# Kernel optimization log

Measured on AMD Instinct MI355X. Metric: run time of the kernel, lower is better.

## Reference

```python
import jax, jax.numpy as jnp
import numpy as np

B, L, D, HD, DC = 2, 2048, 2048, 64, 2048
NH = D // HD  # 32 heads


def _rms_norm(x, eps):
    return x * jax.lax.rsqrt(jnp.mean(jnp.square(x), axis=-1, keepdims=True) + eps)


def _apply_rope(x, rope):
    # x: [b,h,l,d]; rope: [2,l,d]. x_hat = interleave(-x_odd, x_even)
    x2 = x.reshape(*x.shape[:-1], HD // 2, 2)
    x_hat = jnp.stack([-x2[..., 1], x2[..., 0]], axis=-1).reshape(x.shape)
    return x * rope[0] + x_hat * rope[1]


def setup_inputs() -> dict:
    key = jax.random.key(0)
    ks = jax.random.split(key, 6)
    return {
        "x": jax.random.normal(ks[0], (B, L, D), jnp.float32),
        "condition": jax.random.normal(ks[1], (B, DC), jnp.float32),
        "rope": jax.random.normal(ks[2], (2, L, HD), jnp.float32),
        "w_ada": jax.random.normal(ks[3], (2 * D, DC), jnp.float32) * 0.02,
        "w_qkv": jax.random.normal(ks[4], (3 * D, D), jnp.float32) * 0.02,
        "w_out": jax.random.normal(ks[5], (D, D), jnp.float32) * 0.02,
        "qk_w": jnp.ones((HD,), jnp.float32),
    }


def reference(x, condition, rope, w_ada, w_qkv, w_out, qk_w):
    eps = jnp.finfo(x.dtype).eps
    # AdaRMSNorm
    ss = (condition @ w_ada.T)[:, None, :]          # [b,1,2D]
    shift, scale = jnp.split(ss, 2, axis=-1)
    h = _rms_norm(x, eps) * (1.0 + scale) + shift   # [b,l,D]
    # fused QKV projection: 'b l (n h d)'
    qkv = (h @ w_qkv.T).reshape(B, L, 3, NH, HD)
    qkv = jnp.transpose(qkv, (2, 0, 3, 1, 4))       # [3,b,h,l,d]
    q, k, v = qkv[0], qkv[1], qkv[2]
    # per-head RMSNorm (with affine weight) + RoPE
    q = _apply_rope(_rms_norm(q, eps) * qk_w, rope)
    k = _apply_rope(_rms_norm(k, eps) * qk_w, rope)
    # SDPA
    scores = jnp.einsum('bhqd,bhkd->bhqk', q, k) / jnp.sqrt(jnp.asarray(HD, x.dtype))
    attn = jax.nn.softmax(scores, axis=-1)
    o = jnp.einsum('bhqk,bhkd->bhqd', attn, v)      # [b,h,l,d]
    o = jnp.transpose(o, (0, 2, 1, 3)).reshape(B, L, D)
    return o @ w_out.T
```

## Files before the change

kernel.cpp:

```cpp
#include <hip/hip_runtime.h>


typedef __bf16 bf16x8 __attribute__((ext_vector_type(8)));
typedef float  f32x4  __attribute__((ext_vector_type(4)));
typedef float  f32x16 __attribute__((ext_vector_type(16)));

#define EPS_F32 1.1920929e-07f
#define QSCALE 0.18033688011112042f

#if defined(__has_builtin)
#  if __has_builtin(__builtin_amdgcn_exp2f)
#    define EXP2F(x) __builtin_amdgcn_exp2f(x)
#  else
#    define EXP2F(x) __expf((x) * 0.6931471805599453f)
#  endif
#  if __has_builtin(__builtin_amdgcn_rcpf)
#    define RCPF(x) __builtin_amdgcn_rcpf(x)
#  else
#    define RCPF(x) (1.0f / (x))
#  endif
#else
#  define EXP2F(x) __expf((x) * 0.6931471805599453f)
#  define RCPF(x) (1.0f / (x))
#endif

__device__ __forceinline__ float bf2f(unsigned int u16) {
  union { unsigned int i; float f; } v; v.i = (u16 & 0xffffu) << 16; return v.f;
}
__device__ __forceinline__ unsigned short f2bf(float f) {
  union { float f; unsigned int i; } v; v.f = f;
  unsigned int r = v.i + 0x7fffu + ((v.i >> 16) & 1u);
  return (unsigned short)(r >> 16);
}
__device__ __forceinline__ unsigned int f2bf_rn_u(float f) {
  union { float f; unsigned int i; } v; v.f = f;
  return v.i + 0x8000u;
}

__device__ __forceinline__ void gload16(const void* g, void* l) {
  __builtin_amdgcn_global_load_lds(
      (const __attribute__((address_space(1))) unsigned int*)(unsigned long long)g,
      (__attribute__((address_space(3))) unsigned int*)(unsigned int)(unsigned long long)l,
      16, 0, 0);
}

__global__ __launch_bounds__(256) void ada_gemm_kernel(
    const float* __restrict__ cond, const float* __restrict__ w_ada,
    float* __restrict__ ss)
{
  const int lane = threadIdx.x & 63;
  const int gw = blockIdx.x * 4 + (threadIdx.x >> 6);
  const int b = gw >> 12;
  const int j = gw & 4095;
  const float4* wr = (const float4*)(w_ada + j * 2048);
  const float4* cr = (const float4*)(cond + b * 2048);
  float acc = 0.f;
  #pragma unroll
  for (int k4 = 0; k4 < 8; ++k4) {
    float4 w = wr[lane + k4 * 64];
    float4 c = cr[lane + k4 * 64];
    acc += w.x * c.x + w.y * c.y + w.z * c.z + w.w * c.w;
  }
  #pragma unroll
  for (int off = 1; off < 64; off <<= 1) acc += __shfl_xor(acc, off);
  if (lane == 0) ss[b * 4096 + j] = acc;
}

__global__ __launch_bounds__(256) void ada_rms_kernel(
    const float* __restrict__ x, const float* __restrict__ ss,
    unsigned short* __restrict__ H)
{
  const int row = blockIdx.x;
  const int b = row >> 11;
  const int tid = threadIdx.x;
  const int lane = tid & 63, wave = tid >> 6;
  const float* xr = x + (size_t)row * 2048;
  float4 v0 = ((const float4*)xr)[tid * 2];
  float4 v1 = ((const float4*)xr)[tid * 2 + 1];
  float ssq = v0.x*v0.x + v0.y*v0.y + v0.z*v0.z + v0.w*v0.w
            + v1.x*v1.x + v1.y*v1.y + v1.z*v1.z + v1.w*v1.w;
  #pragma unroll
  for (int off = 1; off < 64; off <<= 1) ssq += __shfl_xor(ssq, off);
  __shared__ float red[4];
  if (lane == 0) red[wave] = ssq;
  __syncthreads();
  const float tot = red[0] + red[1] + red[2] + red[3];
  const float r = rsqrtf(tot * (1.f / 2048.f) + EPS_F32);
  const int c0 = tid * 8;
  const float* sh = ss + b * 4096;
  float xv[8] = {v0.x, v0.y, v0.z, v0.w, v1.x, v1.y, v1.z, v1.w};
  unsigned int pk[4];
  #pragma unroll
  for (int p = 0; p < 4; ++p) {
    const int c = c0 + p * 2;
    float h0 = xv[p*2+0] * r * (1.f + sh[2048 + c])     + sh[c];
    float h1 = xv[p*2+1] * r * (1.f + sh[2048 + c + 1]) + sh[c + 1];
    pk[p] = (unsigned int)f2bf(h0) | ((unsigned int)f2bf(h1) << 16);
  }
  *(uint4*)&H[(size_t)row * 2048 + c0] = make_uint4(pk[0], pk[1], pk[2], pk[3]);
}

__global__ __launch_bounds__(256) void cast2_kernel(
    const float* __restrict__ a,
    const float* __restrict__ b,
    unsigned short* __restrict__ dst)
{
  const int i = blockIdx.x * 256 + threadIdx.x;
  float4 v = (i < 3145728) ? ((const float4*)a)[i]
                           : ((const float4*)b)[i - 3145728];
  unsigned int p0 = (unsigned int)f2bf(v.x) | ((unsigned int)f2bf(v.y) << 16);
  unsigned int p1 = (unsigned int)f2bf(v.z) | ((unsigned int)f2bf(v.w) << 16);
  *(uint2*)&dst[(size_t)i * 4] = make_uint2(p0, p1);
}

template <int MODE>
__global__ __launch_bounds__(256) void gemm_bt_kernel(
    const unsigned short* __restrict__ A,
    const unsigned short* __restrict__ Bw,
    void* __restrict__ Cv,
    unsigned short* __restrict__ vt,
    int M, int N, int K)
{
  __shared__ unsigned short As[128 * 32];
  __shared__ unsigned short Bs[128 * 32];
  const int tid  = threadIdx.x;
  const int lane = tid & 63;
  const int wave = tid >> 6;
  const int wm = (wave >> 1) * 64;
  const int wn = (wave & 1) * 64;
  const int bm = blockIdx.y * 128;
  const int bn = blockIdx.x * 128;

  f32x4 acc[4][4] = {};

  const int sm = tid >> 2;
  const int sk = (tid & 3) * 8;
  const unsigned short* Ap  = A  + (size_t)(bm + sm) * K + sk;
  const unsigned short* Ap2 = Ap + (size_t)64 * K;
  const unsigned short* Bp  = Bw + (size_t)(bn + sm) * K + sk;
  const unsigned short* Bp2 = Bp + (size_t)64 * K;
  unsigned short* lA  = &As[tid * 8];
  unsigned short* lA2 = &As[tid * 8 + 2048];
  unsigned short* lB  = &Bs[tid * 8];
  unsigned short* lB2 = &Bs[tid * 8 + 2048];

  const int fr = lane & 15;
  const int fk = (lane >> 4) * 8;

  for (int k0 = 0; k0 < K; k0 += 32) {
    __syncthreads();
    gload16(Ap  + k0, lA);
    gload16(Ap2 + k0, lA2);
    gload16(Bp  + k0, lB);
    gload16(Bp2 + k0, lB2);
    __syncthreads();

    bf16x8 af[4], bfr[4];
    #pragma unroll
    for (int i = 0; i < 4; ++i)
      af[i] = *(const bf16x8*)&As[(wm + i * 16 + fr) * 32 + fk];
    #pragma unroll
    for (int j = 0; j < 4; ++j)
      bfr[j] = *(const bf16x8*)&Bs[(wn + j * 16 + fr) * 32 + fk];
    #pragma unroll
    for (int i = 0; i < 4; ++i)
      #pragma unroll
      for (int j = 0; j < 4; ++j)
        acc[i][j] = __builtin_amdgcn_mfma_f32_16x16x32_bf16(af[i], bfr[j], acc[i][j], 0, 0, 0);
  }

  const int cr = (lane >> 4) * 4;
  const int cc = lane & 15;
  if (MODE == 2 && bn >= 4096) {
    #pragma unroll
    for (int i = 0; i < 4; ++i)
      #pragma unroll
      for (int j = 0; j < 4; ++j)
        #pragma unroll
        for (int r = 0; r < 4; ++r) {
          const int m  = bm + wm + i * 16 + cr + r;
          const int dg = bn + wn + j * 16 + cc - 4096;
          const int l  = m & 2047;
          const size_t dst = ((size_t)((m >> 11) * 32 + (dg >> 6)) * 64 + (dg & 63)) * 2048
                           + (l >> 6) * 64 + (l & 15) * 4 + ((l >> 4) & 3);
          vt[dst] = f2bf(acc[i][j][r]);
        }
  } else {
    #pragma unroll
    for (int i = 0; i < 4; ++i)
      #pragma unroll
      for (int j = 0; j < 4; ++j)
        #pragma unroll
        for (int r = 0; r < 4; ++r) {
          const int row = bm + wm + i * 16 + cr + r;
          const int col = bn + wn + j * 16 + cc;
          if (MODE != 0)
            ((unsigned short*)Cv)[(size_t)row * N + col] = f2bf(acc[i][j][r]);
          else
            ((float*)Cv)[(size_t)row * N + col] = acc[i][j][r];
        }
  }
}

__global__ __launch_bounds__(256) void qk_rope_kernel(
    unsigned short* __restrict__ QKV, const float* __restrict__ rope,
    const float* __restrict__ qk_w)
{
  const int lane = threadIdx.x & 63;
  const int gid = blockIdx.x * 4 + (threadIdx.x >> 6);
  const int l = gid & 2047;
  const int h = (gid >> 11) & 31;
  const int b = gid >> 16;
  const int base = (b * 2048 + l) * 6144 + h * 64 + lane;
  const float r0 = rope[l * 64 + lane];
  const float r1 = rope[131072 + l * 64 + lane];
  const float w  = qk_w[lane];
  #pragma unroll
  for (int t = 0; t < 2; ++t) {
    const int idx = base + 2048 * t;
    const float v = bf2f(QKV[idx]);
    float sq = v * v;
    #pragma unroll
    for (int off = 1; off < 64; off <<= 1) sq += __shfl_xor(sq, off);
    const float vn = v * rsqrtf(sq * (1.f / 64.f) + EPS_F32) * w;
    const float vp = __shfl_xor(vn, 1);
    const float vh = (lane & 1) ? vp : -vp;
    const float scale = (t == 0) ? QSCALE : 1.0f;
    QKV[idx] = f2bf((vn * r0 + vh * r1) * scale);
  }
}

__global__ __launch_bounds__(256, 2) void attn_mfma_kernel(
    const unsigned short* __restrict__ QKV,
    const unsigned short* __restrict__ Vt,
    unsigned short* __restrict__ O)
{
  __shared__ unsigned short Ks[64 * 72];
  __shared__ unsigned short Vs[64 * 72];
  __shared__ unsigned short Ps[4 * 64 * 68];
  const int tid  = threadIdx.x;
  const int lane = tid & 63;
  const int wave = tid >> 6;
  const int blk = blockIdx.x;
  const int bh = blk & 63;
  const int qt = blk >> 6;
  const int b = bh >> 5, h = bh & 31;
  const int rowbase = b << 11;
  const int qbase = qt * 256 + wave * 64;

  const int m16  = lane & 15;
  const int quad = lane >> 4;
  const int m32  = lane & 31;
  const int hl   = lane >> 5;

  bf16x8 qf[4][2];
  #pragma unroll
  for (int qi = 0; qi < 4; ++qi)
    #pragma unroll
    for (int ch = 0; ch < 2; ++ch)
      qf[qi][ch] = *(const bf16x8*)&QKV[(size_t)(rowbase + qbase + qi * 16 + m16) * 6144
                                        + h * 64 + ch * 32 + quad * 8];

  const int sr = tid >> 2;
  const int sc = (tid & 3) * 16;
  const unsigned short* Kg = QKV + (size_t)(rowbase + sr) * 6144 + 2048 + h * 64 + sc;
  const unsigned short* Vg = Vt + (size_t)(bh * 64 + sr) * 2048 + sc;

  f32x16 accO[2][2] = {};
  float part[4][4] = {};
  unsigned short* Pw = &Ps[(wave * 64) * 68];

  for (int kt = 0; kt < 32; ++kt) {
    __syncthreads();
    {
      const uint4* kp = (const uint4*)(Kg + (size_t)kt * 64 * 6144);
      const uint4* vp = (const uint4*)(Vg + kt * 64);
      uint4 k0 = kp[0], k1 = kp[1];
      uint4 v0 = vp[0], v1 = vp[1];
      *(uint4*)&Ks[sr * 72 + sc]     = k0;
      *(uint4*)&Ks[sr * 72 + sc + 8] = k1;
      *(uint4*)&Vs[sr * 72 + sc]     = v0;
      *(uint4*)&Vs[sr * 72 + sc + 8] = v1;
    }
    __syncthreads();

    unsigned int pk[4][4][2];
    #pragma unroll
    for (int kj = 0; kj < 4; ++kj) {
      bf16x8 kf0 = *(const bf16x8*)&Ks[(kj * 16 + m16) * 72 + quad * 8];
      bf16x8 kf1 = *(const bf16x8*)&Ks[(kj * 16 + m16) * 72 + 32 + quad * 8];
      #pragma unroll
      for (int qi = 0; qi < 4; ++qi) {
        f32x4 acc = {};
        acc = __builtin_amdgcn_mfma_f32_16x16x32_bf16(qf[qi][0], kf0, acc, 0, 0, 0);
        acc = __builtin_amdgcn_mfma_f32_16x16x32_bf16(qf[qi][1], kf1, acc, 0, 0, 0);
        #pragma unroll
        for (int r = 0; r < 4; ++r) {
          float p = EXP2F(acc[r]);
          part[qi][r] += p;
          unsigned int pb = f2bf_rn_u(p);
          if (kj == 0)      pk[qi][r][0]  = pb >> 16;
          else if (kj == 1) pk[qi][r][0] |= pb & 0xffff0000u;
          else if (kj == 2) pk[qi][r][1]  = pb >> 16;
          else              pk[qi][r][1] |= pb & 0xffff0000u;
        }
      }
    }
    #pragma unroll
    for (int qi = 0; qi < 4; ++qi)
      #pragma unroll
      for (int r = 0; r < 4; ++r)
        *(uint2*)&Pw[(qi * 16 + quad * 4 + r) * 68 + m16 * 4] =
            make_uint2(pk[qi][r][0], pk[qi][r][1]);

    #pragma unroll
    for (int ch = 0; ch < 4; ++ch) {
      bf16x8 pa0 = *(const bf16x8*)&Pw[m32 * 68 + ch * 16 + hl * 8];
      bf16x8 pa1 = *(const bf16x8*)&Pw[(32 + m32) * 68 + ch * 16 + hl * 8];
      bf16x8 vb0 = *(const bf16x8*)&Vs[m32 * 72 + ch * 16 + hl * 8];
      bf16x8 vb1 = *(const bf16x8*)&Vs[(32 + m32) * 72 + ch * 16 + hl * 8];
      accO[0][0] = __builtin_amdgcn_mfma_f32_32x32x16_bf16(pa0, vb0, accO[0][0], 0, 0, 0);
      accO[0][1] = __builtin_amdgcn_mfma_f32_32x32x16_bf16(pa0, vb1, accO[0][1], 0, 0, 0);
      accO[1][0] = __builtin_amdgcn_mfma_f32_32x32x16_bf16(pa1, vb0, accO[1][0], 0, 0, 0);
      accO[1][1] = __builtin_amdgcn_mfma_f32_32x32x16_bf16(pa1, vb1, accO[1][1], 0, 0, 0);
    }
  }

  #pragma unroll
  for (int qi = 0; qi < 4; ++qi)
    #pragma unroll
    for (int r = 0; r < 4; ++r)
      #pragma unroll
      for (int off = 1; off < 16; off <<= 1)
        part[qi][r] += __shfl_xor(part[qi][r], off);

  #pragma unroll
  for (int qs = 0; qs < 2; ++qs) {
    #pragma unroll
    for (int reg = 0; reg < 16; ++reg) {
      const int r = reg & 3;
      const int s = reg >> 2;
      const int qsrc = ((2 * s + hl) & 3) * 16 + m16;
      const float rs = __shfl(part[qs * 2 + (reg >> 3)][r], qsrc);
      const float inv = RCPF(rs);
      const int rho = r + 8 * s + 4 * hl;
      const size_t base = (size_t)(rowbase + qbase + qs * 32 + rho) * 2048 + h * 64;
      O[base + m32]      = f2bf(accO[qs][0][reg] * inv);
      O[base + 32 + m32] = f2bf(accO[qs][1][reg] * inv);
    }
  }
}

extern "C" void kernel_launch(void* const* d_in, const int* in_sizes, int n_in,
                              void* d_out, int out_size, void* d_ws, size_t ws_size,
                              hipStream_t stream) {
  (void)in_sizes; (void)n_in; (void)out_size; (void)ws_size;
  const float* x     = (const float*)d_in[0];
  const float* cond  = (const float*)d_in[1];
  const float* rope  = (const float*)d_in[2];
  const float* w_ada = (const float*)d_in[3];
  const float* w_qkv = (const float*)d_in[4];
  const float* w_out = (const float*)d_in[5];
  const float* qk_w  = (const float*)d_in[6];
  float* out = (float*)d_out;

  char* ws = (char*)d_ws;
  float*          ss   = (float*)ws;
  unsigned short* H    = (unsigned short*)(ws + 32768);
  unsigned short* Wq   = H + 8388608;
  unsigned short* Wo   = Wq + 12582912;
  unsigned short* QKV  = Wo + 4194304;
  unsigned short* Vt_g = QKV + 25165824;

  ada_gemm_kernel<<<2048, 256, 0, stream>>>(cond, w_ada, ss);
  ada_rms_kernel<<<4096, 256, 0, stream>>>(x, ss, H);
  cast2_kernel<<<16384, 256, 0, stream>>>(w_qkv, w_out, Wq);
  gemm_bt_kernel<2><<<dim3(48, 32), 256, 0, stream>>>(H, Wq, (void*)QKV, Vt_g, 4096, 6144, 2048);
  qk_rope_kernel<<<32768, 256, 0, stream>>>(QKV, rope, qk_w);
  attn_mfma_kernel<<<512, 256, 0, stream>>>(QKV, Vt_g, H);
  gemm_bt_kernel<0><<<dim3(16, 32), 256, 0, stream>>>(H, Wo, (void*)out, nullptr, 4096, 2048, 2048);
}
```

Measured before the change: 477.8 us.

## Fuse QK RMSNorm+RoPE into QKV GEMM epilogue and double-buffer attention K/V

Removes the separate qk_rope kernel by computing the per-head RMSNorm, qk weight, QSCALE and RoPE inside the QKV GEMM epilogue, using a cross-lane shuffle reduction over the 64-wide head tile. Rope is pre-interleaved into float2 pairs in the cast kernel. The V-transpose epilogue now packs four values per 8-byte store instead of scalar scattered stores. The attention kernel double-buffers K/V tiles in shared memory, prefetching the next tile into registers during compute to cut one barrier per iteration. This costs extra LDS and register pressure in attention and a heavier GEMM epilogue.

```diff
diff --git a/kernel.cpp b/kernel.cpp
--- a/kernel.cpp
+++ b/kernel.cpp
@@ -103,14 +103,22 @@
 __global__ __launch_bounds__(256) void cast2_kernel(
     const float* __restrict__ a,
     const float* __restrict__ b,
-    unsigned short* __restrict__ dst)
+    const float* __restrict__ rope,
+    unsigned short* __restrict__ dst,
+    float2* __restrict__ rope2)
 {
-  const int i = blockIdx.x * 256 + threadIdx.x;
-  float4 v = (i < 3145728) ? ((const float4*)a)[i]
-                           : ((const float4*)b)[i - 3145728];
-  unsigned int p0 = (unsigned int)f2bf(v.x) | ((unsigned int)f2bf(v.y) << 16);
-  unsigned int p1 = (unsigned int)f2bf(v.z) | ((unsigned int)f2bf(v.w) << 16);
-  *(uint2*)&dst[(size_t)i * 4] = make_uint2(p0, p1);
+  const int blk = blockIdx.x;
+  if (blk < 16384) {
+    const int i = blk * 256 + threadIdx.x;
+    float4 v = (i < 3145728) ? ((const float4*)a)[i]
+                             : ((const float4*)b)[i - 3145728];
+    unsigned int p0 = (unsigned int)f2bf(v.x) | ((unsigned int)f2bf(v.y) << 16);
+    unsigned int p1 = (unsigned int)f2bf(v.z) | ((unsigned int)f2bf(v.w) << 16);
+    *(uint2*)&dst[(size_t)i * 4] = make_uint2(p0, p1);
+  } else {
+    const int i2 = (blk - 16384) * 256 + threadIdx.x;
+    rope2[i2] = make_float2(rope[i2], rope[131072 + i2]);
+  }
 }
 
 template <int MODE>
@@ -119,6 +127,8 @@
     const unsigned short* __restrict__ Bw,
     void* __restrict__ Cv,
     unsigned short* __restrict__ vt,
+    const float* __restrict__ qk_w,
+    const float2* __restrict__ rope2,
     int M, int N, int K)
 {
   __shared__ unsigned short As[128 * 32];
@@ -169,74 +179,76 @@
         acc[i][j] = __builtin_amdgcn_mfma_f32_16x16x32_bf16(af[i], bfr[j], acc[i][j], 0, 0, 0);
   }
 
-  const int cr = (lane >> 4) * 4;
-  const int cc = lane & 15;
+  const int quad = lane >> 4;
+  const int cc   = lane & 15;
+  const int cr   = quad * 4;
+
   if (MODE == 2 && bn >= 4096) {
+    const int b2 = bm >> 11;
+    const int lb = (bm & 2047) + wm;
+    #pragma unroll
+    for (int j = 0; j < 4; ++j) {
+      const int dg = bn + wn + j * 16 + cc - 4096;
+      unsigned short* vrow = vt + ((size_t)((b2 * 32 + (dg >> 6)) * 64) + (dg & 63)) * 2048;
+      #pragma unroll
+      for (int r = 0; r < 4; ++r) {
+        unsigned int u0 = (unsigned int)f2bf(acc[0][j][r]) | ((unsigned int)f2bf(acc[1][j][r]) << 16);
+        unsigned int u1 = (unsigned int)f2bf(acc[2][j][r]) | ((unsigned int)f2bf(acc[3][j][r]) << 16);
+        *(uint2*)&vrow[lb + (cr + r) * 4] = make_uint2(u0, u1);
+      }
+    }
+  } else if (MODE == 2) {
+    const bool isq = (bn < 2048);
+    float qkw4[4];
+    #pragma unroll
+    for (int j = 0; j < 4; ++j)
+      qkw4[j] = qk_w[j * 16 + cc] * (isq ? QSCALE : 1.0f);
+    unsigned short* C = (unsigned short*)Cv;
+    #pragma unroll
+    for (int i = 0; i < 4; ++i) {
+      #pragma unroll
+      for (int r = 0; r < 4; ++r) {
+        float s2 = acc[0 + 0][0][0] * 0.f;
+        s2 = acc[i][0][r] * acc[i][0][r] + acc[i][1][r] * acc[i][1][r]
+           + acc[i][2][r] * acc[i][2][r] + acc[i][3][r] * acc[i][3][r];
+        s2 += __shfl_xor(s2, 1);
+        s2 += __shfl_xor(s2, 2);
+        s2 += __shfl_xor(s2, 4);
+        s2 += __shfl_xor(s2, 8);
+        const float irms = rsqrtf(s2 * (1.f / 64.f) + EPS_F32);
+        const int m = bm + wm + i * 16 + cr + r;
+        const int l = m & 2047;
+        const float2* rp = rope2 + (size_t)l * 64;
+        #pragma unroll
+        for (int j = 0; j < 4; ++j) {
+          const float vn = acc[i][j][r] * irms * qkw4[j];
+          const float vp = __shfl_xor(vn, 1);
+          const float vh = (cc & 1) ? vp : -vp;
+          const float2 rr = rp[j * 16 + cc];
+          C[(size_t)m * N + bn + wn + j * 16 + cc] = f2bf(vn * rr.x + vh * rr.y);
+        }
+      }
+    }
+  } else {
+    float* C = (float*)Cv;
     #pragma unroll
     for (int i = 0; i < 4; ++i)
       #pragma unroll
       for (int j = 0; j < 4; ++j)
         #pragma unroll
-        for (int r = 0; r < 4; ++r) {
-          const int m  = bm + wm + i * 16 + cr + r;
-          const int dg = bn + wn + j * 16 + cc - 4096;
-          const int l  = m & 2047;
-          const size_t dst = ((size_t)((m >> 11) * 32 + (dg >> 6)) * 64 + (dg & 63)) * 2048
-                           + (l >> 6) * 64 + (l & 15) * 4 + ((l >> 4) & 3);
-          vt[dst] = f2bf(acc[i][j][r]);
-        }
-  } else {
-    #pragma unroll
-    for (int i = 0; i < 4; ++i)
-      #pragma unroll
-      for (int j = 0; j < 4; ++j)
-        #pragma unroll
-        for (int r = 0; r < 4; ++r) {
-          const int row = bm + wm + i * 16 + cr + r;
-          const int col = bn + wn + j * 16 + cc;
-          if (MODE != 0)
-            ((unsigned short*)Cv)[(size_t)row * N + col] = f2bf(acc[i][j][r]);
-          else
-            ((float*)Cv)[(size_t)row * N + col] = acc[i][j][r];
-        }
-  }
-}
-
-__global__ __launch_bounds__(256) void qk_rope_kernel(
-    unsigned short* __restrict__ QKV, const float* __restrict__ rope,
-    const float* __restrict__ qk_w)
-{
-  const int lane = threadIdx.x & 63;
-  const int gid = blockIdx.x * 4 + (threadIdx.x >> 6);
-  const int l = gid & 2047;
-  const int h = (gid >> 11) & 31;
-  const int b = gid >> 16;
-  const int base = (b * 2048 + l) * 6144 + h * 64 + lane;
-  const float r0 = rope[l * 64 + lane];
-  const float r1 = rope[131072 + l * 64 + lane];
-  const float w  = qk_w[lane];
-  #pragma unroll
-  for (int t = 0; t < 2; ++t) {
-    const int idx = base + 2048 * t;
-    const float v = bf2f(QKV[idx]);
-    float sq = v * v;
-    #pragma unroll
-    for (int off = 1; off < 64; off <<= 1) sq += __shfl_xor(sq, off);
-    const float vn = v * rsqrtf(sq * (1.f / 64.f) + EPS_F32) * w;
-    const float vp = __shfl_xor(vn, 1);
-    const float vh = (lane & 1) ? vp : -vp;
-    const float scale = (t == 0) ? QSCALE : 1.0f;
-    QKV[idx] = f2bf((vn * r0 + vh * r1) * scale);
-  }
-}
-
+        for (int r = 0; r < 4; ++r)
+          C[(size_t)(bm + wm + i * 16 + cr + r) * N + bn + wn + j * 16 + cc] = acc[i][j][r];
+  }
+}
+
+#define KVSZ (64 * 72)
 __global__ __launch_bounds__(256, 2) void attn_mfma_kernel(
     const unsigned short* __restrict__ QKV,
     const unsigned short* __restrict__ Vt,
     unsigned short* __restrict__ O)
 {
-  __shared__ unsigned short Ks[64 * 72];
-  __shared__ unsigned short Vs[64 * 72];
+  __shared__ unsigned short Kb[2 * KVSZ];
+  __shared__ unsigned short Vb[2 * KVSZ];
   __shared__ unsigned short Ps[4 * 64 * 68];
   const int tid  = threadIdx.x;
   const int lane = tid & 63;
@@ -270,25 +282,33 @@
   float part[4][4] = {};
   unsigned short* Pw = &Ps[(wave * 64) * 68];
 
+  {
+    const uint4* kp = (const uint4*)Kg;
+    const uint4* vp = (const uint4*)Vg;
+    uint4 k0 = kp[0], k1 = kp[1], v0 = vp[0], v1 = vp[1];
+    *(uint4*)&Kb[sr * 72 + sc]     = k0;
+    *(uint4*)&Kb[sr * 72 + sc + 8] = k1;
+    *(uint4*)&Vb[sr * 72 + sc]     = v0;
+    *(uint4*)&Vb[sr * 72 + sc + 8] = v1;
+  }
+  __syncthreads();
+
   for (int kt = 0; kt < 32; ++kt) {
-    __syncthreads();
-    {
-      const uint4* kp = (const uint4*)(Kg + (size_t)kt * 64 * 6144);
-      const uint4* vp = (const uint4*)(Vg + kt * 64);
-      uint4 k0 = kp[0], k1 = kp[1];
-      uint4 v0 = vp[0], v1 = vp[1];
-      *(uint4*)&Ks[sr * 72 + sc]     = k0;
-      *(uint4*)&Ks[sr * 72 + sc + 8] = k1;
-      *(uint4*)&Vs[sr * 72 + sc]     = v0;
-      *(uint4*)&Vs[sr * 72 + sc + 8] = v1;
-    }
-    __syncthreads();
+    const int cur = kt & 1;
+    uint4 ka, kb2, va, vb2;
+    if (kt < 31) {
+      const uint4* kp = (const uint4*)(Kg + (size_t)(kt + 1) * 64 * 6144);
+      const uint4* vp = (const uint4*)(Vg + (kt + 1) * 64);
+      ka = kp[0]; kb2 = kp[1]; va = vp[0]; vb2 = vp[1];
+    }
+    const unsigned short* Ksc = &Kb[cur * KVSZ];
+    const unsigned short* Vsc = &Vb[cur * KVSZ];
 
     unsigned int pk[4][4][2];
     #pragma unroll
     for (int kj = 0; kj < 4; ++kj) {
-      bf16x8 kf0 = *(const bf16x8*)&Ks[(kj * 16 + m16) * 72 + quad * 8];
-      bf16x8 kf1 = *(const bf16x8*)&Ks[(kj * 16 + m16) * 72 + 32 + quad * 8];
+      bf16x8 kf0 = *(const bf16x8*)&Ksc[(kj * 16 + m16) * 72 + quad * 8];
+      bf16x8 kf1 = *(const bf16x8*)&Ksc[(kj * 16 + m16) * 72 + 32 + quad * 8];
       #pragma unroll
       for (int qi = 0; qi < 4; ++qi) {
         f32x4 acc = {};
@@ -317,13 +337,23 @@
     for (int ch = 0; ch < 4; ++ch) {
       bf16x8 pa0 = *(const bf16x8*)&Pw[m32 * 68 + ch * 16 + hl * 8];
       bf16x8 pa1 = *(const bf16x8*)&Pw[(32 + m32) * 68 + ch * 16 + hl * 8];
-      bf16x8 vb0 = *(const bf16x8*)&Vs[m32 * 72 + ch * 16 + hl * 8];
-      bf16x8 vb1 = *(const bf16x8*)&Vs[(32 + m32) * 72 + ch * 16 + hl * 8];
+      bf16x8 vb0 = *(const bf16x8*)&Vsc[m32 * 72 + ch * 16 + hl * 8];
+      bf16x8 vb1 = *(const bf16x8*)&Vsc[(32 + m32) * 72 + ch * 16 + hl * 8];
       accO[0][0] = __builtin_amdgcn_mfma_f32_32x32x16_bf16(pa0, vb0, accO[0][0], 0, 0, 0);
       accO[0][1] = __builtin_amdgcn_mfma_f32_32x32x16_bf16(pa0, vb1, accO[0][1], 0, 0, 0);
       accO[1][0] = __builtin_amdgcn_mfma_f32_32x32x16_bf16(pa1, vb0, accO[1][0], 0, 0, 0);
       accO[1][1] = __builtin_amdgcn_mfma_f32_32x32x16_bf16(pa1, vb1, accO[1][1], 0, 0, 0);
     }
+
+    if (kt < 31) {
+      unsigned short* Ksn = &Kb[(1 - cur) * KVSZ];
+      unsigned short* Vsn = &Vb[(1 - cur) * KVSZ];
+      *(uint4*)&Ksn[sr * 72 + sc]     = ka;
+      *(uint4*)&Ksn[sr * 72 + sc + 8] = kb2;
+      *(uint4*)&Vsn[sr * 72 + sc]     = va;
+      *(uint4*)&Vsn[sr * 72 + sc + 8] = vb2;
+    }
+    __syncthreads();
   }
 
   #pragma unroll
@@ -371,12 +401,14 @@
   unsigned short* Wo   = Wq + 12582912;
   unsigned short* QKV  = Wo + 4194304;
   unsigned short* Vt_g = QKV + 25165824;
+  float2*         rope2 = (float2*)(Vt_g + 8388608);
 
   ada_gemm_kernel<<<2048, 256, 0, stream>>>(cond, w_ada, ss);
   ada_rms_kernel<<<4096, 256, 0, stream>>>(x, ss, H);
-  cast2_kernel<<<16384, 256, 0, stream>>>(w_qkv, w_out, Wq);
-  gemm_bt_kernel<2><<<dim3(48, 32), 256, 0, stream>>>(H, Wq, (void*)QKV, Vt_g, 4096, 6144, 2048);
-  qk_rope_kernel<<<32768, 256, 0, stream>>>(QKV, rope, qk_w);
+  cast2_kernel<<<16896, 256, 0, stream>>>(w_qkv, w_out, rope, Wq, rope2);
+  gemm_bt_kernel<2><<<dim3(48, 32), 256, 0, stream>>>(
+      H, Wq, (void*)QKV, Vt_g, qk_w, rope2, 4096, 6144, 2048);
   attn_mfma_kernel<<<512, 256, 0, stream>>>(QKV, Vt_g, H);
-  gemm_bt_kernel<0><<<dim3(16, 32), 256, 0, stream>>>(H, Wo, (void*)out, nullptr, 4096, 2048, 2048);
-}
+  gemm_bt_kernel<0><<<dim3(16, 32), 256, 0, stream>>>(
+      H, Wo, (void*)out, nullptr, nullptr, nullptr, 4096, 2048, 2048);
+}
```

After: 495.4 us. +3.7%, slower.

## Double-buffer K/V tiles with async LDS loads and XOR swizzle in attention

Applied to the files above, without the earlier changes.

The attention kernel now issues direct global-to-LDS loads (gload16) for the next K/V tile into a second buffer while the current tile is being computed. Padded LDS rows are replaced by an XOR-swizzled layout to avoid bank conflicts, and the per-iteration syncs are cut to one. The QKV GEMM's V-transpose epilogue also changes to packed 8-byte stores instead of scattered 2-byte stores. This adds LDS usage and relies on the swizzle and the async loads being ordered correctly by the single barrier.

```diff
diff --git a/kernel.cpp b/kernel.cpp
--- a/kernel.cpp
+++ b/kernel.cpp
@@ -169,36 +169,43 @@
         acc[i][j] = __builtin_amdgcn_mfma_f32_16x16x32_bf16(af[i], bfr[j], acc[i][j], 0, 0, 0);
   }
 
-  const int cr = (lane >> 4) * 4;
-  const int cc = lane & 15;
+  const int quad = lane >> 4;
+  const int cc   = lane & 15;
+  const int cr   = quad * 4;
+
   if (MODE == 2 && bn >= 4096) {
+    const int b2 = bm >> 11;
+    const int lb = (bm & 2047) + wm;
+    #pragma unroll
+    for (int j = 0; j < 4; ++j) {
+      const int dg = bn + wn + j * 16 + cc - 4096;
+      unsigned short* vrow = vt + ((size_t)((b2 * 32 + (dg >> 6)) * 64) + (dg & 63)) * 2048;
+      #pragma unroll
+      for (int r = 0; r < 4; ++r) {
+        unsigned int u0 = (unsigned int)f2bf(acc[0][j][r]) | ((unsigned int)f2bf(acc[1][j][r]) << 16);
+        unsigned int u1 = (unsigned int)f2bf(acc[2][j][r]) | ((unsigned int)f2bf(acc[3][j][r]) << 16);
+        *(uint2*)&vrow[lb + (cr + r) * 4] = make_uint2(u0, u1);
+      }
+    }
+  } else if (MODE == 2) {
+    unsigned short* C = (unsigned short*)Cv;
     #pragma unroll
     for (int i = 0; i < 4; ++i)
       #pragma unroll
       for (int j = 0; j < 4; ++j)
         #pragma unroll
-        for (int r = 0; r < 4; ++r) {
-          const int m  = bm + wm + i * 16 + cr + r;
-          const int dg = bn + wn + j * 16 + cc - 4096;
-          const int l  = m & 2047;
-          const size_t dst = ((size_t)((m >> 11) * 32 + (dg >> 6)) * 64 + (dg & 63)) * 2048
-                           + (l >> 6) * 64 + (l & 15) * 4 + ((l >> 4) & 3);
-          vt[dst] = f2bf(acc[i][j][r]);
-        }
+        for (int r = 0; r < 4; ++r)
+          C[(size_t)(bm + wm + i * 16 + cr + r) * N + bn + wn + j * 16 + cc] =
+              f2bf(acc[i][j][r]);
   } else {
+    float* C = (float*)Cv;
     #pragma unroll
     for (int i = 0; i < 4; ++i)
       #pragma unroll
       for (int j = 0; j < 4; ++j)
         #pragma unroll
-        for (int r = 0; r < 4; ++r) {
-          const int row = bm + wm + i * 16 + cr + r;
-          const int col = bn + wn + j * 16 + cc;
-          if (MODE != 0)
-            ((unsigned short*)Cv)[(size_t)row * N + col] = f2bf(acc[i][j][r]);
-          else
-            ((float*)Cv)[(size_t)row * N + col] = acc[i][j][r];
-        }
+        for (int r = 0; r < 4; ++r)
+          C[(size_t)(bm + wm + i * 16 + cr + r) * N + bn + wn + j * 16 + cc] = acc[i][j][r];
   }
 }
 
@@ -230,13 +237,14 @@
   }
 }
 
+#define KVSZ (64 * 64)
 __global__ __launch_bounds__(256, 2) void attn_mfma_kernel(
     const unsigned short* __restrict__ QKV,
     const unsigned short* __restrict__ Vt,
     unsigned short* __restrict__ O)
 {
-  __shared__ unsigned short Ks[64 * 72];
-  __shared__ unsigned short Vs[64 * 72];
+  __shared__ unsigned short Kb[2 * KVSZ];
+  __shared__ unsigned short Vb[2 * KVSZ];
   __shared__ unsigned short Ps[4 * 64 * 68];
   const int tid  = threadIdx.x;
   const int lane = tid & 63;
@@ -261,34 +269,54 @@
       qf[qi][ch] = *(const bf16x8*)&QKV[(size_t)(rowbase + qbase + qi * 16 + m16) * 6144
                                         + h * 64 + ch * 32 + quad * 8];
 
-  const int sr = tid >> 2;
-  const int sc = (tid & 3) * 16;
-  const unsigned short* Kg = QKV + (size_t)(rowbase + sr) * 6144 + 2048 + h * 64 + sc;
-  const unsigned short* Vg = Vt + (size_t)(bh * 64 + sr) * 2048 + sc;
+  const int srow0 = wave * 16 + (lane >> 3);
+  const int sch   = lane & 7;
+  const int kc0 = (sch ^ (srow0 & 7)) * 8;
+  const int kc1 = (sch ^ ((srow0 + 8) & 7)) * 8;
+  const unsigned short* Kg0 = QKV + (size_t)(rowbase + srow0) * 6144 + 2048 + h * 64 + kc0;
+  const unsigned short* Kg1 = QKV + (size_t)(rowbase + srow0 + 8) * 6144 + 2048 + h * 64 + kc1;
+  const unsigned short* Vg0 = Vt + (size_t)(bh * 64 + srow0) * 2048 + kc0;
+  const unsigned short* Vg1 = Vt + (size_t)(bh * 64 + srow0 + 8) * 2048 + kc1;
+  unsigned short* lK0[2] = { &Kb[(wave * 16) * 64 + (lane & 7) * 8 + ((lane >> 3) & 1) * 512],
+                             nullptr };
+  (void)lK0;
 
   f32x16 accO[2][2] = {};
   float part[4][4] = {};
   unsigned short* Pw = &Ps[(wave * 64) * 68];
 
+  const int ldsW = wave * 16 * 64 + lane * 8;
+
+  gload16(Kg0, &Kb[ldsW]);
+  gload16(Kg1, &Kb[ldsW + 512]);
+  gload16(Vg0, &Vb[ldsW]);
+  gload16(Vg1, &Vb[ldsW + 512]);
+  __syncthreads();
+
+  const int x7 = m16 & 7;
+  const int kq0 = (quad ^ x7) * 8;
+  const int kq1 = ((quad ^ x7) ^ 4) * 8;
+  const int y7 = m32 & 7;
+
   for (int kt = 0; kt < 32; ++kt) {
-    __syncthreads();
-    {
-      const uint4* kp = (const uint4*)(Kg + (size_t)kt * 64 * 6144);
-      const uint4* vp = (const uint4*)(Vg + kt * 64);
-      uint4 k0 = kp[0], k1 = kp[1];
-      uint4 v0 = vp[0], v1 = vp[1];
-      *(uint4*)&Ks[sr * 72 + sc]     = k0;
-      *(uint4*)&Ks[sr * 72 + sc + 8] = k1;
-      *(uint4*)&Vs[sr * 72 + sc]     = v0;
-      *(uint4*)&Vs[sr * 72 + sc + 8] = v1;
+    const int cur = kt & 1;
+    if (kt < 31) {
+      const int nb = (1 - cur) * KVSZ;
+      const size_t ko = (size_t)(kt + 1) * 64 * 6144;
+      const int    vo = (kt + 1) * 64;
+      gload16(Kg0 + ko, &Kb[nb + ldsW]);
+      gload16(Kg1 + ko, &Kb[nb + ldsW + 512]);
+      gload16(Vg0 + vo, &Vb[nb + ldsW]);
+      gload16(Vg1 + vo, &Vb[nb + ldsW + 512]);
     }
-    __syncthreads();
+    const unsigned short* Ksc = &Kb[cur * KVSZ];
+    const unsigned short* Vsc = &Vb[cur * KVSZ];
 
     unsigned int pk[4][4][2];
     #pragma unroll
     for (int kj = 0; kj < 4; ++kj) {
-      bf16x8 kf0 = *(const bf16x8*)&Ks[(kj * 16 + m16) * 72 + quad * 8];
-      bf16x8 kf1 = *(const bf16x8*)&Ks[(kj * 16 + m16) * 72 + 32 + quad * 8];
+      bf16x8 kf0 = *(const bf16x8*)&Ksc[(kj * 16 + m16) * 64 + kq0];
+      bf16x8 kf1 = *(const bf16x8*)&Ksc[(kj * 16 + m16) * 64 + kq1];
       #pragma unroll
       for (int qi = 0; qi < 4; ++qi) {
         f32x4 acc = {};
@@ -315,15 +343,18 @@
 
     #pragma unroll
     for (int ch = 0; ch < 4; ++ch) {
+      const int vc = ((2 * ch + hl) ^ y7) * 8;
       bf16x8 pa0 = *(const bf16x8*)&Pw[m32 * 68 + ch * 16 + hl * 8];
       bf16x8 pa1 = *(const bf16x8*)&Pw[(32 + m32) * 68 + ch * 16 + hl * 8];
-      bf16x8 vb0 = *(const bf16x8*)&Vs[m32 * 72 + ch * 16 + hl * 8];
-      bf16x8 vb1 = *(const bf16x8*)&Vs[(32 + m32) * 72 + ch * 16 + hl * 8];
+      bf16x8 vb0 = *(const bf16x8*)&Vsc[m32 * 64 + vc];
+      bf16x8 vb1 = *(const bf16x8*)&Vsc[(32 + m32) * 64 + vc];
       accO[0][0] = __builtin_amdgcn_mfma_f32_32x32x16_bf16(pa0, vb0, accO[0][0], 0, 0, 0);
       accO[0][1] = __builtin_amdgcn_mfma_f32_32x32x16_bf16(pa0, vb1, accO[0][1], 0, 0, 0);
       accO[1][0] = __builtin_amdgcn_mfma_f32_32x32x16_bf16(pa1, vb0, accO[1][0], 0, 0, 0);
       accO[1][1] = __builtin_amdgcn_mfma_f32_32x32x16_bf16(pa1, vb1, accO[1][1], 0, 0, 0);
     }
+
+    __syncthreads();
   }
 
   #pragma unroll
```

Measured after the change: 491.2 us. 2.8% more time.
